# Kernel tuning notes

Measured on AMD Instinct MI355X. Metric: run time of the kernel, lower is better.

The kernel has to match this reference:

```python
import jax, jax.numpy as jnp
import numpy as np
import math

# ---- sizes (must match setup_inputs) ----
D = 256          # distribution dim
K = 2 * D        # parameters per embedding: mean + hidden (log) variance
L = 64           # classes present in batch
B = 8            # samples per class (B_total = B*L = 512)
S = 16           # config['sample_size']
C = 64           # num_classes
LOG_EPS = -100.0
LOG2PI = math.log(2.0 * math.pi)

# ---- NormalDistribution (diagonal, exp parametrization) helpers ----

def _split(p):
    # (..., K) -> mean (..., D), hidden log-variance (..., D)
    return p[..., :D], p[..., D:]


def _logpdf(params, x):
    m, h = _split(params)
    return -0.5 * jnp.sum(LOG2PI + h + (x - m) ** 2 * jnp.exp(-h), axis=-1)


def _logmls(p1, p2):
    # log int N(x; m1, v1) N(x; m2, v2) dx = log N(m1; m2, v1 + v2)
    m1, h1 = _split(p1)
    m2, h2 = _split(p2)
    v = jnp.exp(h1) + jnp.exp(h2)
    return -0.5 * jnp.sum(LOG2PI + jnp.log(v) + (m1 - m2) ** 2 / v, axis=-1)


def _pdf_product(p1, p2):
    # product of two diagonal Gaussians -> new Gaussian params (broadcasting)
    m1, h1 = _split(p1)
    m2, h2 = _split(p2)
    v1, v2 = jnp.exp(h1), jnp.exp(h2)
    vs = v1 + v2
    v = v1 * v2 / vs
    m = (m1 * v2 + m2 * v1) / vs
    return jnp.concatenate(jnp.broadcast_arrays(m, jnp.log(v)), axis=-1)


def _prototypes(support, eps_var):
    # support: (B2, L, K) -> fused prototype params (L, K)
    m, h = _split(support)
    v = eps_var + jnp.exp(h)            # (B2, L, D)
    inv = 1.0 / v
    new_var = 1.0 / inv.sum(0)          # (L, D)
    new_mean = new_var * (m * inv).sum(0)
    new_h = jnp.log(eps_var + new_var)  # ipositive(variance + new_var)
    return jnp.concatenate([new_mean, new_h], axis=-1)


def _compute_logits(query, support, eps_var, key):
    # query: (b, L, K); support: (b2, L, K) -> logits (b, L, L)
    b = query.shape[0]
    protos = _prototypes(support, eps_var)                      # (L, K)
    p = _pdf_product(query[:, :, None, :], protos[None, None])  # (b, L, L, K)
    m, h = _split(p)
    eps = jax.random.normal(key, (b, L, S, L, D), dtype=query.dtype)
    samples = m[:, :, None] + jnp.exp(0.5 * h[:, :, None]) * eps  # (b, L, S, L, D)
    lm = _logmls(query[:, :, None, :], protos[None, None])        # (b, L, L)
    tl = _logpdf(protos[None, None, None], samples)               # (b, L, S, L)
    lse = jax.scipy.special.logsumexp(tl, axis=-1, keepdims=True)  # (b, L, S, 1)
    return lm + jax.scipy.special.logsumexp(-lse, axis=-2) - math.log(S)


def _group_by_class(parameters, labels):
    # balanced labels: each of L labels appears exactly B times
    idx = jnp.argsort(labels)                 # stable in jax
    order = idx.reshape(L, B).T               # (B, L): i-th occurrence of each label
    label_map = labels[idx].reshape(L, B)[:, 0]
    by_class = parameters[idx].reshape(L, B, K).transpose(1, 0, 2)  # (B, L, K)
    return by_class, order, label_map


def setup_inputs() -> dict:
    key = jax.random.key(0)
    k1, k2 = jax.random.split(key)
    parameters = jax.random.normal(k1, (B * L, K), dtype=jnp.float32)
    # balanced labels: each class in [0, L) appears exactly B times, shuffled
    labels = jax.random.permutation(k2, jnp.arange(B * L, dtype=jnp.int32) % L).astype(jnp.int64)
    hidden_epsilon = jnp.asarray(0.01 ** (2.0 / D), dtype=jnp.float32)
    return {"parameters": parameters, "hidden_epsilon": hidden_epsilon, "labels": labels}


def reference(parameters, hidden_epsilon, labels):
    eps_var = jnp.exp(hidden_epsilon)
    by_class, order, label_map = _group_by_class(parameters, labels)
    k = B // 2
    key = jax.random.key(42)
    s1, s2 = jax.random.split(key)
    logits1 = _compute_logits(by_class[:k], by_class[k:], eps_var, s1)
    logits2 = _compute_logits(by_class[k:], by_class[:k], eps_var, s2)
    logits = jnp.concatenate([logits1, logits2], axis=0)          # (B, L, L)
    all_logits = jnp.full((B, L, C), LOG_EPS, dtype=logits.dtype)
    all_logits = all_logits.at[:, :, label_map].set(logits)       # scatter on class dim
    all_logits = all_logits.reshape(B * L, C)
    return all_logits[jnp.argsort(order.reshape(-1))]             # unsort to input order
```

## Files before the change

### kernel.cpp

```cpp
#include <hip/hip_runtime.h>
#include <math.h>

#define DD 256
#define KK 512
#define LL 64
#define BB 8
#define SS 16
#define F_LOG2PI 1.83787706641f
#define PER_I 16777216u

struct U2 { unsigned x, y; };

__host__ __device__ constexpr U2 tf2x32(unsigned k0, unsigned k1, unsigned c0, unsigned c1) {
  unsigned ks2 = k0 ^ k1 ^ 0x1BD11BDAu;
  unsigned x0 = c0 + k0;
  unsigned x1 = c1 + k1;
#define TFR(r) { x0 += x1; x1 = (x1 << (r)) | (x1 >> (32 - (r))); x1 ^= x0; }
  TFR(13) TFR(15) TFR(26) TFR(6)   x0 += k1;  x1 += ks2 + 1u;
  TFR(17) TFR(29) TFR(16) TFR(24)  x0 += ks2; x1 += k0 + 2u;
  TFR(13) TFR(15) TFR(26) TFR(6)   x0 += k0;  x1 += k1 + 3u;
  TFR(17) TFR(29) TFR(16) TFR(24)  x0 += k1;  x1 += ks2 + 4u;
  TFR(13) TFR(15) TFR(26) TFR(6)   x0 += ks2; x1 += k0 + 5u;
#undef TFR
  return U2{x0, x1};
}

__device__ inline unsigned rotl(unsigned x, unsigned r) {
  return __builtin_amdgcn_alignbit(x, x, 32u - r);
}

__device__ inline unsigned tf_fold(unsigned k0, unsigned k1, unsigned x1) {
  unsigned ks2 = k0 ^ k1 ^ 0x1BD11BDAu;
  unsigned x0 = k0;
#define TFR(r) { x0 += x1; x1 = rotl(x1, r); x1 ^= x0; }
  TFR(13u) TFR(15u) TFR(26u) TFR(6u)   x0 += k1;  x1 += ks2 + 1u;
  TFR(17u) TFR(29u) TFR(16u) TFR(24u)  x0 += ks2; x1 += k0 + 2u;
  TFR(13u) TFR(15u) TFR(26u) TFR(6u)   x0 += k0;  x1 += k1 + 3u;
  TFR(17u) TFR(29u) TFR(16u) TFR(24u)  x0 += k1;  x1 += ks2 + 4u;
  TFR(13u) TFR(15u) TFR(26u) TFR(6u)   x0 += ks2; x1 += k0 + 5u;
#undef TFR
  return x0 ^ x1;
}

__device__ inline float normal_pu(unsigned b) {
  float two_fp = __uint_as_float((b >> 9) | 0x40000000u);
  float u = fmaxf(-0.99999994f, two_fp - 3.0f);
  float w = -__logf(fmaf(-u, u, 1.0f));
  float wwf = w - 2.5f;
  float pf =            2.81022636e-08f;
  pf = fmaf(pf, wwf,    3.43273939e-07f);
  pf = fmaf(pf, wwf,   -3.5233877e-06f);
  pf = fmaf(pf, wwf,   -4.39150654e-06f);
  pf = fmaf(pf, wwf,    0.00021858087f);
  pf = fmaf(pf, wwf,   -0.00125372503f);
  pf = fmaf(pf, wwf,   -0.00417768164f);
  pf = fmaf(pf, wwf,    0.246640727f);
  pf = fmaf(pf, wwf,    1.50140941f);
  float wwr = __builtin_amdgcn_sqrtf(w) - 3.0f;
  float pr =           -0.000200214257f;
  pr = fmaf(pr, wwr,    0.000100950558f);
  pr = fmaf(pr, wwr,    0.00134934322f);
  pr = fmaf(pr, wwr,   -0.00367342844f);
  pr = fmaf(pr, wwr,    0.00573950773f);
  pr = fmaf(pr, wwr,   -0.0076224613f);
  pr = fmaf(pr, wwr,    0.00943887047f);
  pr = fmaf(pr, wwr,    1.00167406f);
  pr = fmaf(pr, wwr,    2.83297682f);
  float p = (w < 5.0f) ? pf : pr;
  return p * u;
}


__global__ void k_sort(const int* __restrict__ labels, int* __restrict__ pos,
                       int* __restrict__ lmap) {
  __shared__ int lab[512];
  __shared__ int cnt[64];
  __shared__ int mode;
  int t = threadIdx.x;
  int v = labels[t];
  if (t < 64) cnt[t] = 0;
  if (t == 0) mode = 0;
  __syncthreads();
  atomicAdd(&cnt[v & 63], 1);
  __syncthreads();
  if (t < 64 && cnt[t] != 8) mode = 1;
  __syncthreads();
  if (mode) v = labels[2 * t];
  lab[t] = v & 63;
  __syncthreads();
  int c = lab[t];
  int o = 0;
  for (int j = 0; j < t; ++j) o += (lab[j] == c);
  pos[c * 8 + o] = t;
  if (t < 64) lmap[t] = t;
}

__global__ void k_protos(const float* __restrict__ P, const float* __restrict__ he_p,
                         const int* __restrict__ pos, float* __restrict__ pm,
                         float* __restrict__ pe, float4* __restrict__ pq,
                         float* __restrict__ cl) {
  int hb = blockIdx.x;
  int h = hb >> 6, l = hb & 63;
  int d = threadIdx.x;
  float eps_var = expf(he_p[0]);
  int soff = h ? 0 : 4;
  float sinv = 0.f, sminv = 0.f;
#pragma unroll
  for (int j = 0; j < 4; ++j) {
    int row = pos[l * 8 + soff + j];
    float m = P[row * KK + d];
    float hh = P[row * KK + DD + d];
    float vv = eps_var + expf(hh);
    float iv = 1.0f / vv;
    sinv += iv; sminv += m * iv;
  }
  float nv = 1.0f / sinv;
  float nm = nv * sminv;
  float ev = eps_var + nv;
  pm[hb * DD + d] = nm;
  pe[hb * DD + d] = ev;
  float4 rec; rec.x = nm; rec.y = ev; rec.z = 1.0f / ev; rec.w = 0.0f;
  pq[(h * 256 + d) * 64 + l] = rec;
  float t = F_LOG2PI + __logf(ev);
  for (int off = 32; off; off >>= 1) t += __shfl_xor(t, off);
  __shared__ float red[4];
  int w = d >> 6, lane = d & 63;
  if (lane == 0) red[w] = t;
  __syncthreads();
  if (d == 0) cl[hb] = red[0] + red[1] + red[2] + red[3];
}

__global__ void k_lm(const float* __restrict__ P, const int* __restrict__ pos,
                     const float* __restrict__ pm, const float* __restrict__ pe,
                     float* __restrict__ lm) {
  int bb = blockIdx.x;
  int g = bb >> 6, lq = bb & 63;
  int h = g >> 2;
  int d = threadIdx.x;
  int row = pos[lq * 8 + g];
  float mq = P[row * KK + d];
  float vq = expf(P[row * KK + DD + d]);
  __shared__ float part[4][64];
  int w = d >> 6, lane = d & 63;
  for (int lp = 0; lp < 64; ++lp) {
    int pb = (h * 64 + lp) * DD + d;
    float mp = pm[pb], ev = pe[pb];
    float vs = vq + ev;
    float diff = mq - mp;
    float t = __logf(vs) + diff * diff * __builtin_amdgcn_rcpf(vs);
    for (int off = 32; off; off >>= 1) t += __shfl_xor(t, off);
    if (lane == 0) part[w][lp] = t;
  }
  __syncthreads();
  if (d < 64) {
    float s = part[0][d] + part[1][d] + part[2][d] + part[3][d];
    lm[bb * 64 + d] = -0.5f * (256.0f * F_LOG2PI + s);
  }
}

__global__ __launch_bounds__(256) void k_tl(const float* __restrict__ P,
    const int* __restrict__ pos, const float4* __restrict__ pq,
    float* __restrict__ accbuf) {
  constexpr U2 S1 = tf2x32(0u, 42u, 0u, 0u);
  constexpr U2 S2 = tf2x32(0u, 42u, 0u, 1u);
  int bb = blockIdx.x;
  int h = bb >> 10;
  int lq = (bb >> 4) & 63;
  int chunk = bb & 15;
  int t = threadIdx.x;

  __shared__ float2 q[4 * 256];
#pragma unroll
  for (int i = 0; i < 4; ++i) {
    int row = pos[lq * 8 + h * 4 + i];
    float2 rec;
    rec.x = P[row * KK + t];
    rec.y = expf(P[row * KK + DD + t]);
    q[i * 256 + t] = rec;
  }
  __syncthreads();

  int w = t >> 6, lane = t & 63;
  unsigned k0 = h ? S2.x : S1.x;
  unsigned k1 = h ? S2.y : S1.y;
  unsigned ebk = (unsigned)w * PER_I + (unsigned)lq * 262144u +
                 (unsigned)lane * 256u + (unsigned)chunk * 16u + k1;
  const float2* qd = &q[w * 256];
  const float4* pp = pq + (h * 256 + chunk * 16) * 64 + lane;
  int g = h * 4 + w;
  float* dst = accbuf + ((g * 64 + lq) * 16) * 64 + lane;

  float acc[16];
#pragma unroll
  for (int s = 0; s < 16; ++s) acc[s] = 0.0f;

#pragma unroll 1
  for (int dd = 0; dd < 16; ++dd) {
    float4 pr = pp[dd * 64];
    float2 qv = qd[chunk * 16 + dd];
    float vs  = qv.y + pr.y;
    float ivs = __builtin_amdgcn_rcpf(vs);
    float evs = pr.y * ivs;
    float sivp = __builtin_amdgcn_sqrtf(pr.z);
    float A = (qv.x - pr.x) * evs * sivp;
    float S = __builtin_amdgcn_sqrtf(qv.y * evs) * sivp * 1.41421356f;
    unsigned ebkd = ebk + (unsigned)dd;
#pragma unroll
    for (int s = 0; s < 16; ++s) {
      unsigned bits = tf_fold(k0, k1, ebkd + (unsigned)s * 16384u);
      float eps = normal_pu(bits);
      float diff = fmaf(S, eps, A);
      acc[s] = fmaf(diff, diff, acc[s]);
    }
  }
#pragma unroll
  for (int s = 0; s < 16; ++s) atomicAdd(dst + s * 64, acc[s]);
}

__global__ void k_final(const float* __restrict__ lm, const float* __restrict__ accbuf,
                        const float* __restrict__ cl, const int* __restrict__ pos,
                        const int* __restrict__ lmap, float* __restrict__ out) {
  int bb = blockIdx.x;
  int g = bb >> 6, lq = bb & 63;
  int h = g >> 2;
  int t = threadIdx.x, w = t >> 6, lane = t & 63;
  __shared__ float lsebuf[16];
  float clv = cl[h * 64 + lane];
#pragma unroll
  for (int j = 0; j < 4; ++j) {
    int s = w * 4 + j;
    float tlv = -0.5f * (clv + accbuf[(bb * 16 + s) * 64 + lane]);
    float mx = tlv;
    for (int off = 32; off; off >>= 1) mx = fmaxf(mx, __shfl_xor(mx, off));
    float se = expf(tlv - mx);
    for (int off = 32; off; off >>= 1) se += __shfl_xor(se, off);
    if (lane == 0) lsebuf[s] = mx + __logf(se);
  }
  __syncthreads();
  if (t < 64) {
    float a = (t < 16) ? -lsebuf[t] : -INFINITY;
    float mx = a;
    for (int off = 32; off; off >>= 1) mx = fmaxf(mx, __shfl_xor(mx, off));
    float e = (t < 16) ? expf(a - mx) : 0.0f;
    for (int off = 32; off; off >>= 1) e += __shfl_xor(e, off);
    float mc = mx + __logf(e) - 2.7725887f;
    int row = pos[lq * 8 + g];
    out[row * 64 + lmap[t]] = lm[bb * 64 + t] + mc;
  }
}

extern "C" void kernel_launch(void* const* d_in, const int* in_sizes, int n_in,
                              void* d_out, int out_size, void* d_ws, size_t ws_size,
                              hipStream_t stream) {
  (void)in_sizes; (void)n_in; (void)out_size; (void)ws_size;
  const float* P      = (const float*)d_in[0];
  const float* he     = (const float*)d_in[1];
  const int*   labels = (const int*)d_in[2];
  float* out = (float*)d_out;

  float* ws = (float*)d_ws;
  float* accbuf = ws;
  float4* pq = (float4*)(ws + 524288);
  float* pm  = ws + 655360;
  float* pe  = ws + 688128;
  float* cl  = ws + 720896;
  float* lmw = ws + 721024;
  int*   pos = (int*)(ws + 753792);
  int*   lmp = pos + 512;

  hipMemsetAsync(accbuf, 0, 524288 * sizeof(float), stream);
  hipLaunchKernelGGL(k_sort,   dim3(1),    dim3(512), 0, stream, labels, pos, lmp);
  hipLaunchKernelGGL(k_protos, dim3(128),  dim3(256), 0, stream, P, he, pos, pm, pe, pq, cl);
  hipLaunchKernelGGL(k_lm,     dim3(512),  dim3(256), 0, stream, P, pos, pm, pe, lmw);
  hipLaunchKernelGGL(k_tl,     dim3(2048), dim3(256), 0, stream, P, pos, pq, accbuf);
  hipLaunchKernelGGL(k_final,  dim3(512),  dim3(256), 0, stream, lmw, accbuf, cl, pos, lmp, out);
}
```

Baseline: 423.1 us.

## Pack normal inverse-CDF polynomials into v2f FMAs and restructure k_lm per lane

The two polynomial branches of the inverse-erf approximation are evaluated together as packed 2-wide FMAs, so the hardware can use packed FP32 instructions in the hot sampling path of k_tl. k_lm is rewritten to use one 64-thread wave per block, with each lane owning one prototype and looping over all 256 dimensions using the transposed float4 prototype buffer. This removes the per-prototype wave reductions and lets k_protos skip writing its separate mean and variance arrays. The risk is lower parallelism in k_lm and strided float4 loads.

```diff
diff --git a/kernel.cpp b/kernel.cpp
--- a/kernel.cpp
+++ b/kernel.cpp
@@ -8,6 +8,8 @@
 #define SS 16
 #define F_LOG2PI 1.83787706641f
 #define PER_I 16777216u
+
+typedef float v2f __attribute__((ext_vector_type(2)));
 
 struct U2 { unsigned x, y; };
 
@@ -42,31 +44,29 @@
   return x0 ^ x1;
 }
 
+__device__ inline v2f pkfma(v2f a, v2f b, v2f c) {
+#if __has_builtin(__builtin_elementwise_fma)
+  return __builtin_elementwise_fma(a, b, c);
+#else
+  v2f r; r.x = fmaf(a.x, b.x, c.x); r.y = fmaf(a.y, b.y, c.y); return r;
+#endif
+}
+
 __device__ inline float normal_pu(unsigned b) {
   float two_fp = __uint_as_float((b >> 9) | 0x40000000u);
   float u = fmaxf(-0.99999994f, two_fp - 3.0f);
   float w = -__logf(fmaf(-u, u, 1.0f));
-  float wwf = w - 2.5f;
-  float pf =            2.81022636e-08f;
-  pf = fmaf(pf, wwf,    3.43273939e-07f);
-  pf = fmaf(pf, wwf,   -3.5233877e-06f);
-  pf = fmaf(pf, wwf,   -4.39150654e-06f);
-  pf = fmaf(pf, wwf,    0.00021858087f);
-  pf = fmaf(pf, wwf,   -0.00125372503f);
-  pf = fmaf(pf, wwf,   -0.00417768164f);
-  pf = fmaf(pf, wwf,    0.246640727f);
-  pf = fmaf(pf, wwf,    1.50140941f);
-  float wwr = __builtin_amdgcn_sqrtf(w) - 3.0f;
-  float pr =           -0.000200214257f;
-  pr = fmaf(pr, wwr,    0.000100950558f);
-  pr = fmaf(pr, wwr,    0.00134934322f);
-  pr = fmaf(pr, wwr,   -0.00367342844f);
-  pr = fmaf(pr, wwr,    0.00573950773f);
-  pr = fmaf(pr, wwr,   -0.0076224613f);
-  pr = fmaf(pr, wwr,    0.00943887047f);
-  pr = fmaf(pr, wwr,    1.00167406f);
-  pr = fmaf(pr, wwr,    2.83297682f);
-  float p = (w < 5.0f) ? pf : pr;
+  v2f ww; ww.x = w - 2.5f; ww.y = __builtin_amdgcn_sqrtf(w) - 3.0f;
+  v2f p2; p2.x = 2.81022636e-08f; p2.y = -0.000200214257f;
+  p2 = pkfma(p2, ww, (v2f){ 3.43273939e-07f,  0.000100950558f});
+  p2 = pkfma(p2, ww, (v2f){-3.5233877e-06f,   0.00134934322f});
+  p2 = pkfma(p2, ww, (v2f){-4.39150654e-06f, -0.00367342844f});
+  p2 = pkfma(p2, ww, (v2f){ 0.00021858087f,   0.00573950773f});
+  p2 = pkfma(p2, ww, (v2f){-0.00125372503f,  -0.0076224613f});
+  p2 = pkfma(p2, ww, (v2f){-0.00417768164f,   0.00943887047f});
+  p2 = pkfma(p2, ww, (v2f){ 0.246640727f,     1.00167406f});
+  p2 = pkfma(p2, ww, (v2f){ 1.50140941f,      2.83297682f});
+  float p = (w < 5.0f) ? p2.x : p2.y;
   return p * u;
 }
 
@@ -96,8 +96,7 @@
 }
 
 __global__ void k_protos(const float* __restrict__ P, const float* __restrict__ he_p,
-                         const int* __restrict__ pos, float* __restrict__ pm,
-                         float* __restrict__ pe, float4* __restrict__ pq,
+                         const int* __restrict__ pos, float4* __restrict__ pq,
                          float* __restrict__ cl) {
   int hb = blockIdx.x;
   int h = hb >> 6, l = hb & 63;
@@ -117,8 +116,6 @@
   float nv = 1.0f / sinv;
   float nm = nv * sminv;
   float ev = eps_var + nv;
-  pm[hb * DD + d] = nm;
-  pe[hb * DD + d] = ev;
   float4 rec; rec.x = nm; rec.y = ev; rec.z = 1.0f / ev; rec.w = 0.0f;
   pq[(h * 256 + d) * 64 + l] = rec;
   float t = F_LOG2PI + __logf(ev);
@@ -131,31 +128,33 @@
 }
 
 __global__ void k_lm(const float* __restrict__ P, const int* __restrict__ pos,
-                     const float* __restrict__ pm, const float* __restrict__ pe,
-                     float* __restrict__ lm) {
+                     const float4* __restrict__ pq, float* __restrict__ lm) {
   int bb = blockIdx.x;
   int g = bb >> 6, lq = bb & 63;
   int h = g >> 2;
-  int d = threadIdx.x;
+  int lane = threadIdx.x;
+  __shared__ float2 q[256];
   int row = pos[lq * 8 + g];
-  float mq = P[row * KK + d];
-  float vq = expf(P[row * KK + DD + d]);
-  __shared__ float part[4][64];
-  int w = d >> 6, lane = d & 63;
-  for (int lp = 0; lp < 64; ++lp) {
-    int pb = (h * 64 + lp) * DD + d;
-    float mp = pm[pb], ev = pe[pb];
-    float vs = vq + ev;
-    float diff = mq - mp;
-    float t = __logf(vs) + diff * diff * __builtin_amdgcn_rcpf(vs);
-    for (int off = 32; off; off >>= 1) t += __shfl_xor(t, off);
-    if (lane == 0) part[w][lp] = t;
-  }
-  __syncthreads();
-  if (d < 64) {
-    float s = part[0][d] + part[1][d] + part[2][d] + part[3][d];
-    lm[bb * 64 + d] = -0.5f * (256.0f * F_LOG2PI + s);
-  }
+#pragma unroll
+  for (int j = 0; j < 4; ++j) {
+    int d = j * 64 + lane;
+    float2 rec;
+    rec.x = P[row * KK + d];
+    rec.y = expf(P[row * KK + DD + d]);
+    q[d] = rec;
+  }
+  __syncthreads();
+  const float4* pp = pq + h * 256 * 64 + lane;
+  float t = 0.0f;
+#pragma unroll 4
+  for (int d = 0; d < 256; ++d) {
+    float4 pr = pp[d * 64];
+    float2 qv = q[d];
+    float vs = qv.y + pr.y;
+    float diff = qv.x - pr.x;
+    t += __logf(vs) + diff * diff * __builtin_amdgcn_rcpf(vs);
+  }
+  lm[bb * 64 + lane] = -0.5f * (256.0f * F_LOG2PI + t);
 }
 
 __global__ __launch_bounds__(256) void k_tl(const float* __restrict__ P,
@@ -261,17 +260,15 @@
   float* ws = (float*)d_ws;
   float* accbuf = ws;
   float4* pq = (float4*)(ws + 524288);
-  float* pm  = ws + 655360;
-  float* pe  = ws + 688128;
-  float* cl  = ws + 720896;
-  float* lmw = ws + 721024;
-  int*   pos = (int*)(ws + 753792);
+  float* cl  = ws + 655360;
+  float* lmw = ws + 655488;
+  int*   pos = (int*)(ws + 688256);
   int*   lmp = pos + 512;
 
   hipMemsetAsync(accbuf, 0, 524288 * sizeof(float), stream);
   hipLaunchKernelGGL(k_sort,   dim3(1),    dim3(512), 0, stream, labels, pos, lmp);
-  hipLaunchKernelGGL(k_protos, dim3(128),  dim3(256), 0, stream, P, he, pos, pm, pe, pq, cl);
-  hipLaunchKernelGGL(k_lm,     dim3(512),  dim3(256), 0, stream, P, pos, pm, pe, lmw);
+  hipLaunchKernelGGL(k_protos, dim3(128),  dim3(256), 0, stream, P, he, pos, pq, cl);
+  hipLaunchKernelGGL(k_lm,     dim3(512),  dim3(64),  0, stream, P, pos, pq, lmw);
   hipLaunchKernelGGL(k_tl,     dim3(2048), dim3(256), 0, stream, P, pos, pq, accbuf);
   hipLaunchKernelGGL(k_final,  dim3(512),  dim3(256), 0, stream, lmw, accbuf, cl, pos, lmp, out);
 }
```

New measurement: 416.2 us. Within noise of the previous version (-1.6%).
